# Kernel optimization log

Hardware: AMD Instinct MI355X
Metric: run time of the kernel (lower is better)

The kernel has to match this reference:

```python
import jax, jax.numpy as jnp
import numpy as np

K = 3        # kernel_size
STRIDE = 1
PAD = 1
BASIS = 8    # act_fun.get_size()


def cheb_basis(x):
    """Chebyshev polynomial basis T_0..T_{BASIS-1} of tanh(x); appends basis axis."""
    t = jnp.tanh(x)
    polys = [jnp.ones_like(t), t]
    for _ in range(BASIS - 2):
        polys.append(2.0 * t * polys[-1] - polys[-2])
    return jnp.stack(polys, axis=-1)  # (..., BASIS)


def silu(x):
    return x * jax.nn.sigmoid(x)


def unfold(x):
    """torch F.unfold equivalent: (b,c,h,w) -> (b, c, K*K, L), L = ho*wo."""
    b, c, h, w = x.shape
    ho = (h - K + 2 * PAD) // STRIDE + 1
    wo = (w - K + 2 * PAD) // STRIDE + 1
    xp = jnp.pad(x, ((0, 0), (0, 0), (PAD, PAD), (PAD, PAD)))
    pats = [xp[:, :, i:i + STRIDE * ho:STRIDE, j:j + STRIDE * wo:STRIDE]
            for i in range(K) for j in range(K)]
    pats = jnp.stack(pats, axis=2)  # (b, c, K*K, ho, wo)
    return pats.reshape(b, c, K * K, ho * wo), ho, wo


def setup_inputs() -> dict:
    key = jax.random.key(0)
    k1, k2, k3 = jax.random.split(key, 3)
    cin, cout = 64, 64
    x = jax.random.normal(k1, (16, cin, 32, 32), dtype=jnp.float32)
    # xavier_normal_ on (in,out,k^2,1): std = sqrt(2/(fan_in+fan_out)) approx
    w = jax.random.normal(k2, (cin, cout, K * K), dtype=jnp.float32) * jnp.sqrt(2.0 / (cin + cout))
    # normal_(c, 0, 0.1) on (in,out,k^2,1,basis) -> squeeze the broadcast dim
    c = jax.random.normal(k3, (cin, cout, K * K, BASIS), dtype=jnp.float32) * 0.1
    return {"x": x, "w": w, "c": c}


def reference(x, w, c):
    b = x.shape[0]
    pats, ho, wo = unfold(x)          # (b, i, k, l)
    res = silu(pats)                  # residual activation path
    act = cheb_basis(pats)            # (b, i, k, l, s) spline basis
    # sum_i sum_k w[i,o,k] * res[b,i,k,l]
    term1 = jnp.einsum('iok,bikl->bol', w, res)
    # sum_i sum_k sum_s w[i,o,k]*c[i,o,k,s]*act[b,i,k,l,s] (fused, avoids (b,i,o,k,l,s))
    cw = c * w[..., None]             # (i, o, k, s)
    term2 = jnp.einsum('ioks,bikls->bol', cw, act)
    return (term1 + term2).reshape(b, -1, ho, wo)
```

## Files before the change

kernel.cpp:

```cpp
#include <hip/hip_runtime.h>
#include <hip/hip_bf16.h>


#define CIN   64
#define COUT  64
#define HW    32
#define LL    1024
#define NS    8

typedef __attribute__((ext_vector_type(8))) short short8;
typedef __attribute__((ext_vector_type(4))) float f32x4;


__global__ void prep_kernel(const float* __restrict__ w,
                            const float* __restrict__ c,
                            __hip_bfloat16* __restrict__ Wt,
                            float* __restrict__ bias,
                            const float* __restrict__ x,
                            float* __restrict__ dummy) {
    const int bx = blockIdx.x;
    if (bx < 144) {
        const int tid = bx * 256 + threadIdx.x;
        const int i = tid / (9 * COUT);
        const int r = tid - i * 9 * COUT;
        const int k = r / COUT;
        const int o = r - k * COUT;
        const int widx = (i * COUT + o) * 9 + k;
        const float wv = w[widx];
        __hip_bfloat16* dst = Wt + (size_t)tid * NS;
        dst[0] = __float2bfloat16(wv);
#pragma unroll
        for (int s = 1; s < 8; ++s) dst[s] = __float2bfloat16(wv * c[widx * 8 + s]);
        return;
    }
    if (bx < 208) {
        const int o = bx - 144;
        const int i = threadIdx.x;
        if (i >= 64) return;
        float v = 0.f;
#pragma unroll
        for (int k = 0; k < 9; ++k) {
            const int idx = (i * COUT + o) * 9 + k;
            v += w[idx] * c[idx * 8];
        }
#pragma unroll
        for (int off = 32; off > 0; off >>= 1) v += __shfl_down(v, off);
        if (i == 0) bias[o] = v;
        return;
    }
    const int idx = bx - 208;
    const int r  = idx & 7;
    const int m  = idx >> 3;
    const int b  = r + 8 * (m & 1);
    const int ch = m >> 1;
    const float4 v = ((const float4*)(x + (size_t)(b * CIN + ch) * LL))[threadIdx.x];
    const float acc = v.x + v.y + v.z + v.w;
    if (acc == 1.0e-37f) dummy[threadIdx.x] = acc;
}

__global__ __launch_bounds__(512, 4) void kan_fused_kernel(
        const float* __restrict__ x,
        const __hip_bfloat16* __restrict__ Wt,
        const float* __restrict__ bias,
        float* __restrict__ out) {
    __shared__ __align__(16) unsigned short Wlds[26112];

    const int tid   = threadIdx.x;
    const int wv    = tid >> 6;
    const int lane  = tid & 63;
    const int quad  = lane >> 4;
    const int l16   = lane & 15;
    const int kq    = wv >> 1;
    const int oh    = wv & 1;

    const int b   = blockIdx.x;
    const int row = blockIdx.y;

    const unsigned short* WtU = (const unsigned short*)Wt;

    f32x4 acc[2][2];
#pragma unroll
    for (int h = 0; h < 2; ++h)
#pragma unroll
        for (int nt = 0; nt < 2; ++nt) acc[h][nt] = (f32x4){0.f, 0.f, 0.f, 0.f};

    for (int chunk = 0; chunk < 4; ++chunk) {
        const int chbase = kq * 16 + chunk * 4;
        unsigned short* usd = Wlds + (chunk & 1) * 13056 + kq * 3264;

#pragma unroll
        for (int p = 0; p < 4; ++p) {
            const int cell = (p * 2 + oh) * 64 + lane;
            if (cell < 408) {
                const int ch  = cell & 3;
                const int pos = cell >> 2;
                const int r3  = (pos >= 68) ? 2 : ((pos >= 34) ? 1 : 0);
                const int col = pos - r3 * 34;
                const int gy  = row - 1 + r3;
                const int gx  = col - 1;
                union { __hip_bfloat162 h2[4]; float4 f4; unsigned int u[4]; } U;
                if ((unsigned)gy < 32u && (unsigned)gx < 32u) {
                    const float xv = x[((size_t)(b * CIN + chbase + ch) * HW + gy) * HW + gx];
                    const float em  = __expf(-xv);
                    const float res = xv * __builtin_amdgcn_rcpf(1.f + em);
                    const float e2  = __expf(2.f * xv);
                    const float t   = 1.f - 2.f * __builtin_amdgcn_rcpf(e2 + 1.f);
                    const float t2  = t + t;
                    const float T2 = __builtin_fmaf(t2, t,  -1.f);
                    const float T3 = __builtin_fmaf(t2, T2, -t);
                    const float T4 = __builtin_fmaf(t2, T3, -T2);
                    const float T5 = __builtin_fmaf(t2, T4, -T3);
                    const float T6 = __builtin_fmaf(t2, T5, -T4);
                    const float T7 = __builtin_fmaf(t2, T6, -T5);
                    U.h2[0] = __float22bfloat162_rn(make_float2(res, t));
                    U.h2[1] = __float22bfloat162_rn(make_float2(T2, T3));
                    U.h2[2] = __float22bfloat162_rn(make_float2(T4, T5));
                    U.h2[3] = __float22bfloat162_rn(make_float2(T6, T7));
                } else {
                    U.u[0] = 0x00000000u; U.u[1] = 0x0000BF80u;
                    U.u[2] = 0x00003F80u; U.u[3] = 0x0000BF80u;
                }
                *(float4*)(usd + cell * 8) = U.f4;
            }
        }
        __syncthreads();

        const unsigned short* wchunk = WtU +
            ((size_t)(chbase + quad) * 9 * COUT + (oh << 5) + l16) * NS;
#pragma unroll
        for (int kpos = 0; kpos < 9; ++kpos) {
            const int dy = kpos / 3 - 1, dx = kpos % 3 - 1;
            const int posb = (dy + 1) * 34 + (dx + 1);
            short8 af0 = *(const short8*)(usd + ((posb + l16) * 4 + quad) * 8);
            short8 af1 = *(const short8*)(usd + ((posb + 16 + l16) * 4 + quad) * 8);
#pragma unroll
            for (int nt = 0; nt < 2; ++nt) {
                short8 wf = *(const short8*)(wchunk + (kpos * COUT + nt * 16) * NS);
                acc[0][nt] = __builtin_amdgcn_mfma_f32_16x16x32_bf16(wf, af0, acc[0][nt], 0, 0, 0);
                acc[1][nt] = __builtin_amdgcn_mfma_f32_16x16x32_bf16(wf, af1, acc[1][nt], 0, 0, 0);
            }
        }
    }

    __syncthreads();
    float* red = (float*)Wlds;
#pragma unroll
    for (int h = 0; h < 2; ++h)
#pragma unroll
        for (int nt = 0; nt < 2; ++nt)
#pragma unroll
            for (int r = 0; r < 4; ++r) {
                const int p = h * 16 + l16;
                const int o = (oh << 5) + nt * 16 + quad * 4 + r;
                red[(kq * 32 + p) * 65 + o] = acc[h][nt][r];
            }
    __syncthreads();

#pragma unroll
    for (int rep = 0; rep < 4; ++rep) {
        const int v = rep * 512 + tid;
        const int p = v & 31;
        const int o = v >> 5;
        const float s = red[p * 65 + o] + red[(32 + p) * 65 + o]
                      + red[(64 + p) * 65 + o] + red[(96 + p) * 65 + o] + bias[o];
        out[(size_t)(b * COUT + o) * LL + row * HW + p] = s;
    }
}

extern "C" void kernel_launch(void* const* d_in, const int* in_sizes, int n_in,
                              void* d_out, int out_size, void* d_ws, size_t ws_size,
                              hipStream_t stream) {
    const float* x = (const float*)d_in[0];
    const float* w = (const float*)d_in[1];
    const float* c = (const float*)d_in[2];
    float* out = (float*)d_out;

    char* ws = (char*)d_ws;
    __hip_bfloat16* Wt   = (__hip_bfloat16*)(ws);
    float*          bias = (float*)(ws + 589824);
    float*          dummy = (float*)(ws + 590080);

    prep_kernel<<<1232, 256, 0, stream>>>(w, c, Wt, bias, x, dummy);
    kan_fused_kernel<<<dim3(16, 32), 512, 0, stream>>>(x, Wt, bias, out);
}
```

Before: 79.56 us.

## Retile fused KAN conv to two rows per block and split output halves

Each block now computes two output rows for one half of the output channels (grid 16x16x2, 256 threads) instead of one row for all channels. The four-row input halo is expanded into the bf16 basis once and reused by the MFMA tiles of both output rows, which cuts the halo recomputation from three rows per output row to two. In exchange, each output-half block recomputes the basis for the same input, and the block needs more LDS and more accumulator registers. The sigmoid and tanh now share a single exp, and the __syncthreads before the reduction is removed. That removal looks unsafe: it relies on the reduction scratch overlapping only buffer 0, whose last reads happened before chunk 3's barrier, while slower waves may still be reading buffer 1 for chunk 3.

Result: no change. 80.89 us (+1.7%).

```diff
diff --git a/kernel.cpp b/kernel.cpp
--- a/kernel.cpp
+++ b/kernel.cpp
@@ -58,53 +58,52 @@
     if (acc == 1.0e-37f) dummy[threadIdx.x] = acc;
 }
 
-__global__ __launch_bounds__(512, 4) void kan_fused_kernel(
+__global__ __launch_bounds__(256, 2) void kan_fused_kernel(
         const float* __restrict__ x,
         const __hip_bfloat16* __restrict__ Wt,
         const float* __restrict__ bias,
         float* __restrict__ out) {
-    __shared__ __align__(16) unsigned short Wlds[26112];
+    __shared__ __align__(16) unsigned short Wlds[34816];
 
     const int tid   = threadIdx.x;
-    const int wv    = tid >> 6;
+    const int kq    = tid >> 6;
     const int lane  = tid & 63;
     const int quad  = lane >> 4;
     const int l16   = lane & 15;
-    const int kq    = wv >> 1;
-    const int oh    = wv & 1;
 
-    const int b   = blockIdx.x;
-    const int row = blockIdx.y;
+    const int b    = blockIdx.x;
+    const int row0 = blockIdx.y * 2;
+    const int oh   = blockIdx.z;
 
     const unsigned short* WtU = (const unsigned short*)Wt;
 
-    f32x4 acc[2][2];
+    f32x4 acc[4][2];
 #pragma unroll
-    for (int h = 0; h < 2; ++h)
+    for (int h = 0; h < 4; ++h)
 #pragma unroll
         for (int nt = 0; nt < 2; ++nt) acc[h][nt] = (f32x4){0.f, 0.f, 0.f, 0.f};
 
     for (int chunk = 0; chunk < 4; ++chunk) {
         const int chbase = kq * 16 + chunk * 4;
-        unsigned short* usd = Wlds + (chunk & 1) * 13056 + kq * 3264;
+        unsigned short* usd = Wlds + (chunk & 1) * 17408 + kq * 4352;
 
 #pragma unroll
-        for (int p = 0; p < 4; ++p) {
-            const int cell = (p * 2 + oh) * 64 + lane;
-            if (cell < 408) {
+        for (int p = 0; p < 9; ++p) {
+            const int cell = p * 64 + lane;
+            if (cell < 544) {
                 const int ch  = cell & 3;
                 const int pos = cell >> 2;
-                const int r3  = (pos >= 68) ? 2 : ((pos >= 34) ? 1 : 0);
-                const int col = pos - r3 * 34;
-                const int gy  = row - 1 + r3;
+                const int r4  = (pos >= 102) ? 3 : ((pos >= 68) ? 2 : ((pos >= 34) ? 1 : 0));
+                const int col = pos - r4 * 34;
+                const int gy  = row0 - 1 + r4;
                 const int gx  = col - 1;
                 union { __hip_bfloat162 h2[4]; float4 f4; unsigned int u[4]; } U;
                 if ((unsigned)gy < 32u && (unsigned)gx < 32u) {
                     const float xv = x[((size_t)(b * CIN + chbase + ch) * HW + gy) * HW + gx];
-                    const float em  = __expf(-xv);
-                    const float res = xv * __builtin_amdgcn_rcpf(1.f + em);
-                    const float e2  = __expf(2.f * xv);
-                    const float t   = 1.f - 2.f * __builtin_amdgcn_rcpf(e2 + 1.f);
+                    const float e   = __expf(xv);
+                    const float sig = e * __builtin_amdgcn_rcpf(1.f + e);
+                    const float res = xv * sig;
+                    const float t   = 1.f - 2.f * __builtin_amdgcn_rcpf(e * e + 1.f);
                     const float t2  = t + t;
                     const float T2 = __builtin_fmaf(t2, t,  -1.f);
                     const float T3 = __builtin_fmaf(t2, T2, -t);
@@ -130,40 +129,45 @@
 #pragma unroll
         for (int kpos = 0; kpos < 9; ++kpos) {
             const int dy = kpos / 3 - 1, dx = kpos % 3 - 1;
-            const int posb = (dy + 1) * 34 + (dx + 1);
-            short8 af0 = *(const short8*)(usd + ((posb + l16) * 4 + quad) * 8);
-            short8 af1 = *(const short8*)(usd + ((posb + 16 + l16) * 4 + quad) * 8);
+            short8 af[4];
+#pragma unroll
+            for (int hr = 0; hr < 2; ++hr) {
+                const int posb = (1 + hr + dy) * 34 + (1 + dx);
+                af[hr * 2 + 0] = *(const short8*)(usd + ((posb + l16) * 4 + quad) * 8);
+                af[hr * 2 + 1] = *(const short8*)(usd + ((posb + 16 + l16) * 4 + quad) * 8);
+            }
 #pragma unroll
             for (int nt = 0; nt < 2; ++nt) {
                 short8 wf = *(const short8*)(wchunk + (kpos * COUT + nt * 16) * NS);
-                acc[0][nt] = __builtin_amdgcn_mfma_f32_16x16x32_bf16(wf, af0, acc[0][nt], 0, 0, 0);
-                acc[1][nt] = __builtin_amdgcn_mfma_f32_16x16x32_bf16(wf, af1, acc[1][nt], 0, 0, 0);
+#pragma unroll
+                for (int h = 0; h < 4; ++h)
+                    acc[h][nt] = __builtin_amdgcn_mfma_f32_16x16x32_bf16(wf, af[h], acc[h][nt], 0, 0, 0);
             }
         }
     }
 
-    __syncthreads();
     float* red = (float*)Wlds;
 #pragma unroll
-    for (int h = 0; h < 2; ++h)
+    for (int h = 0; h < 4; ++h)
 #pragma unroll
         for (int nt = 0; nt < 2; ++nt)
 #pragma unroll
             for (int r = 0; r < 4; ++r) {
-                const int p = h * 16 + l16;
-                const int o = (oh << 5) + nt * 16 + quad * 4 + r;
-                red[(kq * 32 + p) * 65 + o] = acc[h][nt][r];
+                const int p  = (h >> 1) * 32 + (h & 1) * 16 + l16;
+                const int ol = nt * 16 + quad * 4 + r;
+                red[(kq * 64 + p) * 33 + ol] = acc[h][nt][r];
             }
     __syncthreads();
 
 #pragma unroll
-    for (int rep = 0; rep < 4; ++rep) {
-        const int v = rep * 512 + tid;
-        const int p = v & 31;
-        const int o = v >> 5;
-        const float s = red[p * 65 + o] + red[(32 + p) * 65 + o]
-                      + red[(64 + p) * 65 + o] + red[(96 + p) * 65 + o] + bias[o];
-        out[(size_t)(b * COUT + o) * LL + row * HW + p] = s;
+    for (int rep = 0; rep < 8; ++rep) {
+        const int v  = rep * 256 + tid;
+        const int p  = v & 63;
+        const int ol = v >> 6;
+        const int o  = (oh << 5) + ol;
+        const float s = red[p * 33 + ol] + red[(64 + p) * 33 + ol]
+                      + red[(128 + p) * 33 + ol] + red[(192 + p) * 33 + ol] + bias[o];
+        out[(size_t)(b * COUT + o) * LL + (row0 + (p >> 5)) * HW + (p & 31)] = s;
     }
 }
 
@@ -176,10 +180,10 @@
     float* out = (float*)d_out;
 
     char* ws = (char*)d_ws;
-    __hip_bfloat16* Wt   = (__hip_bfloat16*)(ws);
-    float*          bias = (float*)(ws + 589824);
+    __hip_bfloat16* Wt    = (__hip_bfloat16*)(ws);
+    float*          bias  = (float*)(ws + 589824);
     float*          dummy = (float*)(ws + 590080);
 
     prep_kernel<<<1232, 256, 0, stream>>>(w, c, Wt, bias, x, dummy);
-    kan_fused_kernel<<<dim3(16, 32), 512, 0, stream>>>(x, Wt, bias, out);
+    kan_fused_kernel<<<dim3(16, 16, 2), 256, 0, stream>>>(x, Wt, bias, out);
 }
```

## Stage padded input halo rows in LDS once and compute basis from a single exp

Applied to the files above, without the earlier changes.

At kernel start, each block copies its three-row input halo for all 64 channels into shared memory as fp32, with zero padding. The per-chunk basis build then reads from LDS instead of doing scattered global loads with bounds checks. Padding cells now go through the same math, since x=0 gives the constants the old code hard-wired. Sigmoid and tanh are now both derived from one exp, and the pre-reduction barrier is dropped. Shared memory grows by about 26 KB per block, which can lower how many blocks fit on a CU.

Result: faster. 77.26 us (-2.9%).

```diff
diff --git a/kernel.cpp b/kernel.cpp
--- a/kernel.cpp
+++ b/kernel.cpp
@@ -63,7 +63,7 @@
         const __hip_bfloat16* __restrict__ Wt,
         const float* __restrict__ bias,
         float* __restrict__ out) {
-    __shared__ __align__(16) unsigned short Wlds[26112];
+    __shared__ __align__(16) unsigned short Wlds[39168];
 
     const int tid   = threadIdx.x;
     const int wv    = tid >> 6;
@@ -77,6 +77,25 @@
     const int row = blockIdx.y;
 
     const unsigned short* WtU = (const unsigned short*)Wt;
+    float* xf = (float*)Wlds;
+
+#pragma unroll
+    for (int p = 0; p < 13; ++p) {
+        const int cell = p * 512 + tid;
+        if (cell < 6528) {
+            const int ch  = cell / 102;
+            const int pos = cell - ch * 102;
+            const int r3  = (pos >= 68) ? 2 : ((pos >= 34) ? 1 : 0);
+            const int col = pos - r3 * 34;
+            const int gy  = row - 1 + r3;
+            const int gx  = col - 1;
+            float v = 0.f;
+            if ((unsigned)gy < 32u && (unsigned)gx < 32u)
+                v = x[((size_t)(b * CIN + ch) * HW + gy) * HW + gx];
+            xf[ch * 102 + pos] = v;
+        }
+    }
+    __syncthreads();
 
     f32x4 acc[2][2];
 #pragma unroll
@@ -86,7 +105,7 @@
 
     for (int chunk = 0; chunk < 4; ++chunk) {
         const int chbase = kq * 16 + chunk * 4;
-        unsigned short* usd = Wlds + (chunk & 1) * 13056 + kq * 3264;
+        unsigned short* usd = Wlds + 13056 + (chunk & 1) * 13056 + kq * 3264;
 
 #pragma unroll
         for (int p = 0; p < 4; ++p) {
@@ -94,32 +113,23 @@
             if (cell < 408) {
                 const int ch  = cell & 3;
                 const int pos = cell >> 2;
-                const int r3  = (pos >= 68) ? 2 : ((pos >= 34) ? 1 : 0);
-                const int col = pos - r3 * 34;
-                const int gy  = row - 1 + r3;
-                const int gx  = col - 1;
-                union { __hip_bfloat162 h2[4]; float4 f4; unsigned int u[4]; } U;
-                if ((unsigned)gy < 32u && (unsigned)gx < 32u) {
-                    const float xv = x[((size_t)(b * CIN + chbase + ch) * HW + gy) * HW + gx];
-                    const float em  = __expf(-xv);
-                    const float res = xv * __builtin_amdgcn_rcpf(1.f + em);
-                    const float e2  = __expf(2.f * xv);
-                    const float t   = 1.f - 2.f * __builtin_amdgcn_rcpf(e2 + 1.f);
-                    const float t2  = t + t;
-                    const float T2 = __builtin_fmaf(t2, t,  -1.f);
-                    const float T3 = __builtin_fmaf(t2, T2, -t);
-                    const float T4 = __builtin_fmaf(t2, T3, -T2);
-                    const float T5 = __builtin_fmaf(t2, T4, -T3);
-                    const float T6 = __builtin_fmaf(t2, T5, -T4);
-                    const float T7 = __builtin_fmaf(t2, T6, -T5);
-                    U.h2[0] = __float22bfloat162_rn(make_float2(res, t));
-                    U.h2[1] = __float22bfloat162_rn(make_float2(T2, T3));
-                    U.h2[2] = __float22bfloat162_rn(make_float2(T4, T5));
-                    U.h2[3] = __float22bfloat162_rn(make_float2(T6, T7));
-                } else {
-                    U.u[0] = 0x00000000u; U.u[1] = 0x0000BF80u;
-                    U.u[2] = 0x00003F80u; U.u[3] = 0x0000BF80u;
-                }
+                const float xv = xf[(chbase + ch) * 102 + pos];
+                const float e   = __expf(xv);
+                const float sig = e * __builtin_amdgcn_rcpf(1.f + e);
+                const float res = xv * sig;
+                const float t   = 1.f - 2.f * __builtin_amdgcn_rcpf(__builtin_fmaf(e, e, 1.f));
+                const float t2  = t + t;
+                const float T2 = __builtin_fmaf(t2, t,  -1.f);
+                const float T3 = __builtin_fmaf(t2, T2, -t);
+                const float T4 = __builtin_fmaf(t2, T3, -T2);
+                const float T5 = __builtin_fmaf(t2, T4, -T3);
+                const float T6 = __builtin_fmaf(t2, T5, -T4);
+                const float T7 = __builtin_fmaf(t2, T6, -T5);
+                union { __hip_bfloat162 h2[4]; float4 f4; } U;
+                U.h2[0] = __float22bfloat162_rn(make_float2(res, t));
+                U.h2[1] = __float22bfloat162_rn(make_float2(T2, T3));
+                U.h2[2] = __float22bfloat162_rn(make_float2(T4, T5));
+                U.h2[3] = __float22bfloat162_rn(make_float2(T6, T7));
                 *(float4*)(usd + cell * 8) = U.f4;
             }
         }
@@ -142,7 +152,6 @@
         }
     }
 
-    __syncthreads();
     float* red = (float*)Wlds;
 #pragma unroll
     for (int h = 0; h < 2; ++h)
@@ -176,8 +185,8 @@
     float* out = (float*)d_out;
 
     char* ws = (char*)d_ws;
-    __hip_bfloat16* Wt   = (__hip_bfloat16*)(ws);
-    float*          bias = (float*)(ws + 589824);
+    __hip_bfloat16* Wt    = (__hip_bfloat16*)(ws);
+    float*          bias  = (float*)(ws + 589824);
     float*          dummy = (float*)(ws + 590080);
 
     prep_kernel<<<1232, 256, 0, stream>>>(w, c, Wt, bias, x, dummy);
```
